# Optimization experiments

Hardware: AMD Instinct MI355X
Metric: run time of the kernel (lower is better)

Reference implementation:

```python
import jax, jax.numpy as jnp
import numpy as np

B, T, C = 4, 1024, 768
H, HS = 12, 64           # num_heads, head_size
VD = 2 * HS              # value dim per head


def setup_inputs() -> dict:
    key = jax.random.key(0)
    ks = jax.random.split(key, 16)
    s = 0.02
    inp = {
        "x": jax.random.normal(ks[0], (B, T, C), jnp.float32),
        "Wq1": jax.random.normal(ks[1], (H, C, HS), jnp.float32) * s,
        "Wk1": jax.random.normal(ks[2], (H, C, HS), jnp.float32) * s,
        "Wq2": jax.random.normal(ks[3], (H, C, HS), jnp.float32) * s,
        "Wk2": jax.random.normal(ks[4], (H, C, HS), jnp.float32) * s,
        "Wv": jax.random.normal(ks[5], (H, C, VD), jnp.float32) * s,
        "lq1": jax.random.normal(ks[6], (H, HS), jnp.float32) * 0.1,
        "lk1": jax.random.normal(ks[7], (H, HS), jnp.float32) * 0.1,
        "lq2": jax.random.normal(ks[8], (H, HS), jnp.float32) * 0.1,
        "lk2": jax.random.normal(ks[9], (H, HS), jnp.float32) * 0.1,
        "gn_w": jnp.ones((H * VD,), jnp.float32),
        "gn_b": jnp.zeros((H * VD,), jnp.float32),
        "Wp": jax.random.normal(ks[10], (C, H * VD), jnp.float32) * s,
        "bp": jnp.zeros((C,), jnp.float32),
        "layer_idx": 3,
    }
    return inp


def _diff_attn(x, Wq1, Wk1, Wq2, Wk2, Wv, lq1, lk1, lq2, lk2,
               gn_w, gn_b, Wp, bp, layer_idx):
    Bc, Tc, _ = x.shape
    scale = 1.0 / jnp.sqrt(jnp.float32(HS))
    # per-head projections: [B,H,T,HS]
    q1 = jnp.einsum('btc,hcd->bhtd', x, Wq1)
    k1 = jnp.einsum('btc,hcd->bhtd', x, Wk1)
    q2 = jnp.einsum('btc,hcd->bhtd', x, Wq2)
    k2 = jnp.einsum('btc,hcd->bhtd', x, Wk2)
    v = jnp.einsum('btc,hce->bhte', x, Wv)           # [B,H,T,2HS]
    mask = jnp.tril(jnp.ones((Tc, Tc), bool))         # causal
    neg = jnp.float32(-jnp.inf)
    a1 = jnp.einsum('bhtd,bhsd->bhts', q1, k1) * scale
    a2 = jnp.einsum('bhtd,bhsd->bhts', q2, k2) * scale
    a1 = jax.nn.softmax(jnp.where(mask, a1, neg), axis=-1)
    a2 = jax.nn.softmax(jnp.where(mask, a2, neg), axis=-1)
    # dynamic lambda init, per get_lambda
    li = jnp.float32(layer_idx)
    dyn = 0.8 - 0.6 * jnp.exp(-0.3 * (li - 1.0))
    lam = jnp.mean(jnp.exp(lq1 * lk1) - jnp.exp(lq2 * lk2) + dyn, axis=-1)  # [H]
    diff = a1 - lam[None, :, None, None] * a2
    out = jnp.einsum('bhts,bhse->bhte', diff, v)      # [B,H,T,2HS]
    out = out.transpose(0, 2, 1, 3).reshape(Bc, Tc, H * VD)
    # GroupLayerNorm == full layernorm over last dim (unbiased=False var)
    mu = out.mean(-1, keepdims=True)
    var = jnp.mean((out - mu) ** 2, axis=-1, keepdims=True)
    out = (out - mu) / jnp.sqrt(var + 1e-5) * gn_w + gn_b
    out = out * 0.2  # (1 - lambda_init_buffer=0.8), buffer never updated
    return out @ Wp.T + bp


def reference(x, Wq1, Wk1, Wq2, Wk2, Wv, lq1, lk1, lq2, lk2,
              gn_w, gn_b, Wp, bp, layer_idx):
    return _diff_attn(x, Wq1, Wk1, Wq2, Wk2, Wv, lq1, lk1, lq2, lk2,
                      gn_w, gn_b, Wp, bp, layer_idx)
```

## Files before the change

kernel.cpp:

```cpp
#include <hip/hip_runtime.h>
#include <hip/hip_bf16.h>

#define Bc   4
#define Tc   1024
#define Cc   768
#define Hc   12
#define HSc  64
#define VDc  128
#define NQKV 4608
#define YLD  3072
#define NROWS 4096
#define HVD  1536

#define Q1OFF 0
#define K1OFF 768
#define Q2OFF 1536
#define K2OFF 2304

typedef __bf16 bf16x8 __attribute__((ext_vector_type(8)));
typedef float f32x4 __attribute__((ext_vector_type(4)));

#define PW_S 36
#define EXP2SCALE 0.18033688011112042f

static __device__ __forceinline__ float bf2f(unsigned short s) {
    return __uint_as_float(((unsigned int)s) << 16);
}
static __device__ __forceinline__ unsigned short f2bf(float f) {
    unsigned int u = __float_as_uint(f);
    unsigned int r = (u + 0x7FFFu + ((u >> 16) & 1u)) >> 16;
    return (unsigned short)r;
}
static __device__ __forceinline__ unsigned int pack2bf(float lo, float hi) {
    unsigned int a = (__float_as_uint(lo) + 0x8000u) >> 16;
    unsigned int b = (__float_as_uint(hi) + 0x8000u) & 0xFFFF0000u;
    return a | b;
}

static __device__ __forceinline__ void load16_lds(const void* g, void* l) {
    __builtin_amdgcn_global_load_lds(
        (const __attribute__((address_space(1))) void*)g,
        (__attribute__((address_space(3))) void*)l, 16, 0, 0);
}

__global__ __launch_bounds__(256) void cast_bf16(
    const float* __restrict__ src, unsigned short* __restrict__ dst)
{
    int i = blockIdx.x * 256 + threadIdx.x;
    float4 v = *(const float4*)(src + (size_t)i * 4);
    ushort4 u;
    u.x = f2bf(v.x); u.y = f2bf(v.y); u.z = f2bf(v.z); u.w = f2bf(v.w);
    *(ushort4*)(dst + (size_t)i * 4) = u;
}

__global__ __launch_bounds__(256) void trans_w(
    const float* __restrict__ Wq1, const float* __restrict__ Wk1,
    const float* __restrict__ Wq2, const float* __restrict__ Wk2,
    const float* __restrict__ Wv, unsigned short* __restrict__ WcatT)
{
    __shared__ float tile[64][65];
    int tid = threadIdx.x;
    int t = blockIdx.x;
    int kt = t % 12, nt = t / 12;
    int k0 = kt * 64, n0 = nt * 64;
    const float* src;
    int stride;
    if (n0 < 3072) {
        int which = n0 / 768, m = n0 - which * 768, h = m >> 6;
        const float* W = (which == 0) ? Wq1 : (which == 1) ? Wk1 : (which == 2) ? Wq2 : Wk2;
        src = W + ((size_t)h * 768 + k0) * 64;
        stride = 64;
    } else {
        int rel = n0 - 3072, h = rel >> 7, e0 = rel & 127;
        src = Wv + ((size_t)h * 768 + k0) * 128 + e0;
        stride = 128;
    }
    for (int i = tid; i < 4096; i += 256) {
        int kl = i >> 6, dl = i & 63;
        tile[dl][kl] = src[(size_t)kl * stride + dl];
    }
    __syncthreads();
    for (int i = tid; i < 4096; i += 256) {
        int nl = i >> 6, kl = i & 63;
        WcatT[(size_t)(n0 + nl) * 768 + k0 + kl] = f2bf(tile[nl][kl]);
    }
}

__global__ __launch_bounds__(64) void lambda_kernel(
    const float* __restrict__ lq1, const float* __restrict__ lk1,
    const float* __restrict__ lq2, const float* __restrict__ lk2,
    const int* __restrict__ layer_idx, float* __restrict__ lam)
{
    int h = blockIdx.x, l = threadIdx.x;
    float li = (float)layer_idx[0];
    float dyn = 0.8f - 0.6f * expf(-0.3f * (li - 1.0f));
    int i = h * HSc + l;
    float v = expf(lq1[i] * lk1[i]) - expf(lq2[i] * lk2[i]) + dyn;
    #pragma unroll
    for (int off = 32; off; off >>= 1) v += __shfl_xor(v, off);
    if (l == 0) lam[h] = v * (1.0f / 64.0f);
}

template<int TN, int KD, int LDC, bool OUT_BIAS, bool SPLITV>
__global__ __launch_bounds__(256) void gemm_mfma(
    const unsigned short* __restrict__ A, const unsigned short* __restrict__ Bt,
    unsigned short* __restrict__ Cb, float* __restrict__ Cf,
    const float* __restrict__ bias, unsigned short* __restrict__ VtOut)
{
    constexpr int BN = TN * 32;
    constexpr int JB = TN / 2;
    __shared__ unsigned short As[128 * 32];
    __shared__ unsigned short Bs[BN * 32];
    int tid = threadIdx.x, lane = tid & 63, w = tid >> 6;
    int wm = w >> 1, wn = w & 1;
    int m0 = blockIdx.y * 128, n0 = blockIdx.x * BN;

    int lr = lane >> 2, lq = lane & 3;
    const unsigned short* gA[2];
    const unsigned short* gB[JB];
    #pragma unroll
    for (int j = 0; j < 2; ++j) {
        int row = w * 32 + j * 16 + lr;
        int qg = lq ^ ((row >> 1) & 3);
        gA[j] = A + (size_t)(m0 + row) * KD + qg * 8;
    }
    #pragma unroll
    for (int j = 0; j < JB; ++j) {
        int row = w * (JB * 16) + j * 16 + lr;
        int qg = lq ^ ((row >> 1) & 3);
        gB[j] = Bt + (size_t)(n0 + row) * KD + qg * 8;
    }

    int rr = lane & 15, qd = lane >> 4;
    const unsigned short* aAddr[4];
    const unsigned short* bAddr[TN];
    #pragma unroll
    for (int i = 0; i < 4; ++i) {
        int row = wm * 64 + i * 16 + rr;
        int qs = qd ^ ((row >> 1) & 3);
        aAddr[i] = As + row * 32 + qs * 8;
    }
    #pragma unroll
    for (int t = 0; t < TN; ++t) {
        int row = wn * (TN * 16) + t * 16 + rr;
        int qs = qd ^ ((row >> 1) & 3);
        bAddr[t] = Bs + row * 32 + qs * 8;
    }

    f32x4 acc[4][TN];
    #pragma unroll
    for (int i = 0; i < 4; ++i)
        #pragma unroll
        for (int t = 0; t < TN; ++t) acc[i][t] = {0.f, 0.f, 0.f, 0.f};

    for (int k = 0; k < KD / 32; ++k) {
        __syncthreads();
        load16_lds(gA[0], As + (w * 2 + 0) * 512);
        load16_lds(gA[1], As + (w * 2 + 1) * 512);
        #pragma unroll
        for (int j = 0; j < JB; ++j)
            load16_lds(gB[j], Bs + (w * JB + j) * 512);
        gA[0] += 32; gA[1] += 32;
        #pragma unroll
        for (int j = 0; j < JB; ++j) gB[j] += 32;
        __syncthreads();

        bf16x8 af[4], bfr[TN];
        #pragma unroll
        for (int i = 0; i < 4; ++i) af[i] = *(const bf16x8*)aAddr[i];
        #pragma unroll
        for (int t = 0; t < TN; ++t) bfr[t] = *(const bf16x8*)bAddr[t];
        #pragma unroll
        for (int i = 0; i < 4; ++i)
            #pragma unroll
            for (int t = 0; t < TN; ++t)
                acc[i][t] = __builtin_amdgcn_mfma_f32_16x16x32_bf16(af[i], bfr[t], acc[i][t], 0, 0, 0);
    }

    #pragma unroll
    for (int t = 0; t < TN; ++t) {
        int col = n0 + wn * (TN * 16) + t * 16 + rr;
        if (SPLITV && col >= 3072) {
            int rel = col - 3072, hh = rel >> 7, e = rel & 127;
            #pragma unroll
            for (int i = 0; i < 4; ++i) {
                int row0 = m0 + wm * 64 + i * 16 + qd * 4;
                int b = row0 >> 10, tt = row0 & 1023;
                ushort4 pk;
                pk.x = f2bf(acc[i][t][0]); pk.y = f2bf(acc[i][t][1]);
                pk.z = f2bf(acc[i][t][2]); pk.w = f2bf(acc[i][t][3]);
                *(ushort4*)&VtOut[(size_t)((b * Hc + hh) * 128 + e) * 1024 + tt] = pk;
            }
        } else {
            float bv = OUT_BIAS ? bias[col] : 0.f;
            #pragma unroll
            for (int i = 0; i < 4; ++i) {
                #pragma unroll
                for (int r = 0; r < 4; ++r) {
                    int row = m0 + wm * 64 + i * 16 + qd * 4 + r;
                    if (OUT_BIAS)
                        Cf[(size_t)row * LDC + col] = acc[i][t][r] + bv;
                    else
                        Cb[(size_t)row * LDC + col] = f2bf(acc[i][t][r]);
                }
            }
        }
    }
}

__global__ __launch_bounds__(256) void diff_attn_mfma(
    const unsigned short* __restrict__ Y, const unsigned short* __restrict__ Vt,
    const float* __restrict__ lam_buf, unsigned short* __restrict__ attn)
{
    __shared__ __align__(16) unsigned short KV[2][8192];
    __shared__ __align__(16) unsigned int PL32[4][16 * PW_S];

    int bh = blockIdx.x;
    int b = bh / Hc, h = bh - b * Hc;
    int g = 15 - (int)blockIdx.y;
    int tid = threadIdx.x, lane = tid & 63, wv = tid >> 6;
    int cl = lane & 15, qd = lane >> 4;
    float lamv = lam_buf[h];
    size_t rowbase = (size_t)(b * Tc) * YLD;
    const int hq = h * HSc;
    unsigned int* Pw = PL32[wv];
    const unsigned short* VtB = Vt + ((size_t)bh << 17);
    const f32x4 zero4 = {0.f, 0.f, 0.f, 0.f};

    int ksrow = lane >> 3;
    int ksch  = (lane & 7) ^ ksrow;
    int offk[4];
    {
        int mat = wv & 1;
        int moff = mat ? K2OFF : K1OFF;
        #pragma unroll
        for (int r8 = 0; r8 < 4; ++r8)
            offk[r8] = (r8 * 8 + ksrow) * YLD + moff + hq + ksch * 8;
    }
    int vsel = lane >> 2;
    int vsch = (lane & 3) ^ (vsel & 3);
    int offv[4];
    {
        int sv0 = (wv & 1) * 4;
        #pragma unroll
        for (int i = 0; i < 4; ++i)
            offv[i] = ((sv0 + i) * 16 + vsel) * 1024 + vsch * 8;
    }

    auto stage = [&](int kt, int cur) {
        char* base = (char*)KV[cur] + wv * 4096;
        if (wv < 2) {
            const unsigned short* g0 = Y + rowbase + (size_t)(kt * 32) * YLD;
            #pragma unroll
            for (int r8 = 0; r8 < 4; ++r8)
                load16_lds(g0 + offk[r8], base + r8 * 1024);
        } else {
            const unsigned short* g0 = VtB + kt * 32;
            #pragma unroll
            for (int i = 0; i < 4; ++i)
                load16_lds(g0 + offv[i], base + i * 1024);
        }
    };

    int kfo[2][4], vfo[8];
    #pragma unroll
    for (int c = 0; c < 2; ++c) {
        int row = c * 16 + cl;
        #pragma unroll
        for (int j = 0; j < 4; ++j)
            kfo[c][j] = (j >> 1) * 4096 + row * 128 +
                        ((((j & 1) * 4 + qd) ^ (row & 7)) << 4);
    }
    #pragma unroll
    for (int ec = 0; ec < 8; ++ec) {
        int e = ec * 16 + cl;
        vfo[ec] = 8192 + e * 64 + ((qd ^ (e & 3)) << 4);
    }

    int qrow = g * 64 + wv * 16;

    size_t qoff = rowbase + (size_t)(qrow + cl) * YLD;
    bf16x8 q1a = *(const bf16x8*)(Y + qoff + Q1OFF + hq + qd * 8);
    bf16x8 q1b = *(const bf16x8*)(Y + qoff + Q1OFF + hq + 32 + qd * 8);
    bf16x8 q2a = *(const bf16x8*)(Y + qoff + Q2OFF + hq + qd * 8);
    bf16x8 q2b = *(const bf16x8*)(Y + qoff + Q2OFF + hq + 32 + qd * 8);

    f32x4 O1[8], O2[8];
    #pragma unroll
    for (int ec = 0; ec < 8; ++ec) { O1[ec] = zero4; O2[ec] = zero4; }
    float l1[4] = {0.f, 0.f, 0.f, 0.f}, l2[4] = {0.f, 0.f, 0.f, 0.f};

    auto tile = [&](int cur, int kt, bool diag) {
        const char* kb = (const char*)KV[cur];
        bf16x8 kf[2][4];
        #pragma unroll
        for (int c = 0; c < 2; ++c)
            #pragma unroll
            for (int j = 0; j < 4; ++j)
                kf[c][j] = *(const bf16x8*)(kb + kfo[c][j]);

        f32x4 S1[2], S2[2];
        #pragma unroll
        for (int c = 0; c < 2; ++c) { S1[c] = zero4; S2[c] = zero4; }
        #pragma unroll
        for (int c = 0; c < 2; ++c) {
            S1[c] = __builtin_amdgcn_mfma_f32_16x16x32_bf16(q1a, kf[c][0], S1[c], 0, 0, 0);
            S1[c] = __builtin_amdgcn_mfma_f32_16x16x32_bf16(q1b, kf[c][1], S1[c], 0, 0, 0);
            S2[c] = __builtin_amdgcn_mfma_f32_16x16x32_bf16(q2a, kf[c][2], S2[c], 0, 0, 0);
            S2[c] = __builtin_amdgcn_mfma_f32_16x16x32_bf16(q2b, kf[c][3], S2[c], 0, 0, 0);
        }
        if (diag) {
            #pragma unroll
            for (int c = 0; c < 2; ++c) {
                int kq = kt * 32 + c * 16 + cl - qrow - qd * 4;
                #pragma unroll
                for (int r = 0; r < 4; ++r) {
                    if (kq > r) { S1[c][r] = -1e30f; S2[c][r] = -1e30f; }
                }
            }
        }
        bf16x8 vf[8];
        #pragma unroll
        for (int ec = 0; ec < 8; ++ec)
            vf[ec] = *(const bf16x8*)(kb + vfo[ec]);

        #pragma unroll
        for (int r = 0; r < 4; ++r) {
            float p10 = exp2f(S1[0][r] * EXP2SCALE);
            float p11 = exp2f(S1[1][r] * EXP2SCALE);
            float p20 = exp2f(S2[0][r] * EXP2SCALE);
            float p21 = exp2f(S2[1][r] * EXP2SCALE);
            l1[r] += p10 + p11;
            l2[r] += p20 + p21;
            int row = (qd << 2) + r;
            Pw[row * PW_S + cl]      = pack2bf(p10, p20);
            Pw[row * PW_S + cl + 16] = pack2bf(p11, p21);
        }
        const unsigned int* rp = Pw + cl * PW_S + qd * 8;
        uint4 L0 = *(const uint4*)(rp);
        uint4 L1 = *(const uint4*)(rp + 4);
        uint4 u1, u2;
        u1.x = __builtin_amdgcn_perm(L0.y, L0.x, 0x05040100u);
        u1.y = __builtin_amdgcn_perm(L0.w, L0.z, 0x05040100u);
        u1.z = __builtin_amdgcn_perm(L1.y, L1.x, 0x05040100u);
        u1.w = __builtin_amdgcn_perm(L1.w, L1.z, 0x05040100u);
        u2.x = __builtin_amdgcn_perm(L0.y, L0.x, 0x07060302u);
        u2.y = __builtin_amdgcn_perm(L0.w, L0.z, 0x07060302u);
        u2.z = __builtin_amdgcn_perm(L1.y, L1.x, 0x07060302u);
        u2.w = __builtin_amdgcn_perm(L1.w, L1.z, 0x07060302u);
        bf16x8 pa1 = __builtin_bit_cast(bf16x8, u1);
        bf16x8 pa2 = __builtin_bit_cast(bf16x8, u2);
        #pragma unroll
        for (int ec = 0; ec < 8; ++ec) {
            O1[ec] = __builtin_amdgcn_mfma_f32_16x16x32_bf16(pa1, vf[ec], O1[ec], 0, 0, 0);
            O2[ec] = __builtin_amdgcn_mfma_f32_16x16x32_bf16(pa2, vf[ec], O2[ec], 0, 0, 0);
        }
    };

    int NT = 2 * g + 2;
    int ktmax = 2 * g + (wv >> 1);

    stage(0, 0);
    __syncthreads();
    for (int kt = 0; kt < NT; ++kt) {
        int cur = kt & 1;
        if (kt + 1 < NT) stage(kt + 1, cur ^ 1);
        if (kt <= ktmax) {
            bool diag = (kt * 32 + 31 > qrow);
            tile(cur, kt, diag);
        }
        __syncthreads();
    }

    float w1[4], w2[4];
    #pragma unroll
    for (int r = 0; r < 4; ++r) {
        float a = l1[r], c = l2[r];
        a += __shfl_xor(a, 1); a += __shfl_xor(a, 2);
        a += __shfl_xor(a, 4); a += __shfl_xor(a, 8);
        c += __shfl_xor(c, 1); c += __shfl_xor(c, 2);
        c += __shfl_xor(c, 4); c += __shfl_xor(c, 8);
        w1[r] = 1.0f / a;
        w2[r] = lamv / c;
    }
    #pragma unroll
    for (int ec = 0; ec < 8; ++ec) {
        #pragma unroll
        for (int r = 0; r < 4; ++r) {
            size_t row = (size_t)(b * Tc + qrow + qd * 4 + r);
            attn[row * HVD + h * VDc + ec * 16 + cl] =
                f2bf(O1[ec][r] * w1[r] - O2[ec][r] * w2[r]);
        }
    }
}

__global__ __launch_bounds__(128) void ln_inplace(
    unsigned short* __restrict__ attn,
    const float* __restrict__ gnw, const float* __restrict__ gnb)
{
    int row = blockIdx.x, tid = threadIdx.x;
    unsigned short* p = attn + (size_t)row * HVD;
    float v[12];
    float s = 0.f, sq = 0.f;
    #pragma unroll
    for (int j = 0; j < 3; ++j) {
        int g = tid + j * 128;
        ushort4 u = *(const ushort4*)(p + g * 4);
        float x0 = bf2f(u.x), x1 = bf2f(u.y), x2 = bf2f(u.z), x3 = bf2f(u.w);
        v[j * 4 + 0] = x0; v[j * 4 + 1] = x1; v[j * 4 + 2] = x2; v[j * 4 + 3] = x3;
        s += x0 + x1 + x2 + x3;
        sq = fmaf(x0, x0, sq); sq = fmaf(x1, x1, sq);
        sq = fmaf(x2, x2, sq); sq = fmaf(x3, x3, sq);
    }
    #pragma unroll
    for (int off = 32; off; off >>= 1) { s += __shfl_xor(s, off); sq += __shfl_xor(sq, off); }
    __shared__ float ss[2], sqs[2];
    if ((tid & 63) == 0) { ss[tid >> 6] = s; sqs[tid >> 6] = sq; }
    __syncthreads();
    float S = ss[0] + ss[1], Q = sqs[0] + sqs[1];
    float mu = S * (1.0f / HVD);
    float rstd = rsqrtf(Q * (1.0f / HVD) - mu * mu + 1e-5f);
    #pragma unroll
    for (int j = 0; j < 3; ++j) {
        int g = tid + j * 128;
        float4 gw = *(const float4*)(gnw + g * 4);
        float4 gb = *(const float4*)(gnb + g * 4);
        ushort4 o;
        o.x = f2bf(((v[j * 4 + 0] - mu) * rstd * gw.x + gb.x) * 0.2f);
        o.y = f2bf(((v[j * 4 + 1] - mu) * rstd * gw.y + gb.y) * 0.2f);
        o.z = f2bf(((v[j * 4 + 2] - mu) * rstd * gw.z + gb.z) * 0.2f);
        o.w = f2bf(((v[j * 4 + 3] - mu) * rstd * gw.w + gb.w) * 0.2f);
        *(ushort4*)(p + g * 4) = o;
    }
}

extern "C" void kernel_launch(void* const* d_in, const int* in_sizes, int n_in,
                              void* d_out, int out_size, void* d_ws, size_t ws_size,
                              hipStream_t stream)
{
    const float* x   = (const float*)d_in[0];
    const float* Wq1 = (const float*)d_in[1];
    const float* Wk1 = (const float*)d_in[2];
    const float* Wq2 = (const float*)d_in[3];
    const float* Wk2 = (const float*)d_in[4];
    const float* Wv  = (const float*)d_in[5];
    const float* lq1 = (const float*)d_in[6];
    const float* lk1 = (const float*)d_in[7];
    const float* lq2 = (const float*)d_in[8];
    const float* lk2 = (const float*)d_in[9];
    const float* gnw = (const float*)d_in[10];
    const float* gnb = (const float*)d_in[11];
    const float* Wp  = (const float*)d_in[12];
    const float* bp  = (const float*)d_in[13];
    const int*   lidx = (const int*)d_in[14];
    float* out = (float*)d_out;

    char* w = (char*)d_ws;
    unsigned short* WcatT = (unsigned short*)(w);
    unsigned short* Xb    = (unsigned short*)(w + 7077888);
    unsigned short* Y     = (unsigned short*)(w + 13369344);
    unsigned short* VtW   = (unsigned short*)(w + 38535168);
    unsigned short* attn  = (unsigned short*)(w + 51118080);
    unsigned short* Wpb   = (unsigned short*)(w + 63700992);
    float* lam            = (float*)(w + 66060288);

    cast_bf16<<<dim3(NROWS * Cc / 1024), 256, 0, stream>>>(x, Xb);
    cast_bf16<<<dim3(Cc * HVD / 1024), 256, 0, stream>>>(Wp, Wpb);
    trans_w<<<dim3(72 * 12), 256, 0, stream>>>(Wq1, Wk1, Wq2, Wk2, Wv, WcatT);
    lambda_kernel<<<dim3(Hc), 64, 0, stream>>>(lq1, lk1, lq2, lk2, lidx, lam);
    gemm_mfma<4, 768, YLD, false, true><<<dim3(NQKV / 128, NROWS / 128), 256, 0, stream>>>(
        Xb, WcatT, Y, nullptr, nullptr, VtW);
    diff_attn_mfma<<<dim3(Bc * Hc, 16), 256, 0, stream>>>(Y, VtW, lam, attn);
    ln_inplace<<<dim3(NROWS), 128, 0, stream>>>(attn, gnw, gnb);
    gemm_mfma<2, HVD, Cc, true, false><<<dim3(Cc / 64, NROWS / 128), 256, 0, stream>>>(
        attn, Wpb, nullptr, out, bp, nullptr);
}
```

Baseline: 284.2 us.

## Triple-buffer K/V staging with single barrier and raw v_exp in diff attention

Replaces the double-buffered K/V LDS staging with a three-slot ring that prefetches two tiles ahead. Each iteration uses one explicit vmcnt wait plus s_barrier instead of two __syncthreads. K/V fragments are read into registers before the next stage is issued. The V swizzle pattern changes to reduce LDS bank conflicts, and exp2f is replaced with a raw v_exp_f32. The cost is more LDS per block, which may lower occupancy, and relying on hand-counted vmcnt values adds correctness risk.

```diff
diff --git a/kernel.cpp b/kernel.cpp
--- a/kernel.cpp
+++ b/kernel.cpp
@@ -19,6 +19,7 @@
 
 typedef __bf16 bf16x8 __attribute__((ext_vector_type(8)));
 typedef float f32x4 __attribute__((ext_vector_type(4)));
+typedef unsigned int u32x4 __attribute__((ext_vector_type(4)));
 
 #define PW_S 36
 #define EXP2SCALE 0.18033688011112042f
@@ -35,6 +36,11 @@
     unsigned int a = (__float_as_uint(lo) + 0x8000u) >> 16;
     unsigned int b = (__float_as_uint(hi) + 0x8000u) & 0xFFFF0000u;
     return a | b;
+}
+static __device__ __forceinline__ float fast_exp2(float x) {
+    float r;
+    asm("v_exp_f32 %0, %1" : "=v"(r) : "v"(x));
+    return r;
 }
 
 static __device__ __forceinline__ void load16_lds(const void* g, void* l) {
@@ -212,7 +218,7 @@
     const unsigned short* __restrict__ Y, const unsigned short* __restrict__ Vt,
     const float* __restrict__ lam_buf, unsigned short* __restrict__ attn)
 {
-    __shared__ __align__(16) unsigned short KV[2][8192];
+    __shared__ __align__(16) unsigned short KVring[3 * 8192];
     __shared__ __align__(16) unsigned int PL32[4][16 * PW_S];
 
     int bh = blockIdx.x;
@@ -238,7 +244,7 @@
             offk[r8] = (r8 * 8 + ksrow) * YLD + moff + hq + ksch * 8;
     }
     int vsel = lane >> 2;
-    int vsch = (lane & 3) ^ (vsel & 3);
+    int vsch = (lane & 3) ^ ((vsel >> 1) & 3);
     int offv[4];
     {
         int sv0 = (wv & 1) * 4;
@@ -247,8 +253,8 @@
             offv[i] = ((sv0 + i) * 16 + vsel) * 1024 + vsch * 8;
     }
 
-    auto stage = [&](int kt, int cur) {
-        char* base = (char*)KV[cur] + wv * 4096;
+    auto stage = [&](int kt, int slot) {
+        char* base = (char*)KVring + slot * 16384 + wv * 4096;
         if (wv < 2) {
             const unsigned short* g0 = Y + rowbase + (size_t)(kt * 32) * YLD;
             #pragma unroll
@@ -274,102 +280,114 @@
     #pragma unroll
     for (int ec = 0; ec < 8; ++ec) {
         int e = ec * 16 + cl;
-        vfo[ec] = 8192 + e * 64 + ((qd ^ (e & 3)) << 4);
+        vfo[ec] = 8192 + e * 64 + ((qd ^ ((e >> 1) & 3)) << 4);
     }
 
     int qrow = g * 64 + wv * 16;
 
     size_t qoff = rowbase + (size_t)(qrow + cl) * YLD;
-    bf16x8 q1a = *(const bf16x8*)(Y + qoff + Q1OFF + hq + qd * 8);
-    bf16x8 q1b = *(const bf16x8*)(Y + qoff + Q1OFF + hq + 32 + qd * 8);
-    bf16x8 q2a = *(const bf16x8*)(Y + qoff + Q2OFF + hq + qd * 8);
-    bf16x8 q2b = *(const bf16x8*)(Y + qoff + Q2OFF + hq + 32 + qd * 8);
+    u32x4 uq1a = *(const u32x4*)(Y + qoff + Q1OFF + hq + qd * 8);
+    u32x4 uq1b = *(const u32x4*)(Y + qoff + Q1OFF + hq + 32 + qd * 8);
+    u32x4 uq2a = *(const u32x4*)(Y + qoff + Q2OFF + hq + qd * 8);
+    u32x4 uq2b = *(const u32x4*)(Y + qoff + Q2OFF + hq + 32 + qd * 8);
+    asm volatile("" : "+v"(uq1a), "+v"(uq1b), "+v"(uq2a), "+v"(uq2b));
+    asm volatile("" : "+v"(lamv));
+    asm volatile("s_waitcnt vmcnt(0)" ::: "memory");
+    bf16x8 q1a = __builtin_bit_cast(bf16x8, uq1a);
+    bf16x8 q1b = __builtin_bit_cast(bf16x8, uq1b);
+    bf16x8 q2a = __builtin_bit_cast(bf16x8, uq2a);
+    bf16x8 q2b = __builtin_bit_cast(bf16x8, uq2b);
 
     f32x4 O1[8], O2[8];
     #pragma unroll
     for (int ec = 0; ec < 8; ++ec) { O1[ec] = zero4; O2[ec] = zero4; }
     float l1[4] = {0.f, 0.f, 0.f, 0.f}, l2[4] = {0.f, 0.f, 0.f, 0.f};
 
-    auto tile = [&](int cur, int kt, bool diag) {
-        const char* kb = (const char*)KV[cur];
+    int NT = 2 * g + 2;
+    int ktmax = 2 * g + (wv >> 1);
+
+    stage(0, 0);
+    stage(1, 1);
+
+    int cur = 0;
+    for (int kt = 0; kt < NT; ++kt) {
+        if (kt < NT - 1) {
+            asm volatile("s_waitcnt vmcnt(4)\n\ts_barrier" ::: "memory");
+        } else {
+            asm volatile("s_waitcnt vmcnt(0)\n\ts_barrier" ::: "memory");
+        }
+        const char* kb = (const char*)KVring + cur * 16384;
+
         bf16x8 kf[2][4];
         #pragma unroll
         for (int c = 0; c < 2; ++c)
             #pragma unroll
             for (int j = 0; j < 4; ++j)
                 kf[c][j] = *(const bf16x8*)(kb + kfo[c][j]);
-
-        f32x4 S1[2], S2[2];
-        #pragma unroll
-        for (int c = 0; c < 2; ++c) { S1[c] = zero4; S2[c] = zero4; }
-        #pragma unroll
-        for (int c = 0; c < 2; ++c) {
-            S1[c] = __builtin_amdgcn_mfma_f32_16x16x32_bf16(q1a, kf[c][0], S1[c], 0, 0, 0);
-            S1[c] = __builtin_amdgcn_mfma_f32_16x16x32_bf16(q1b, kf[c][1], S1[c], 0, 0, 0);
-            S2[c] = __builtin_amdgcn_mfma_f32_16x16x32_bf16(q2a, kf[c][2], S2[c], 0, 0, 0);
-            S2[c] = __builtin_amdgcn_mfma_f32_16x16x32_bf16(q2b, kf[c][3], S2[c], 0, 0, 0);
-        }
-        if (diag) {
-            #pragma unroll
-            for (int c = 0; c < 2; ++c) {
-                int kq = kt * 32 + c * 16 + cl - qrow - qd * 4;
-                #pragma unroll
-                for (int r = 0; r < 4; ++r) {
-                    if (kq > r) { S1[c][r] = -1e30f; S2[c][r] = -1e30f; }
-                }
-            }
-        }
         bf16x8 vf[8];
         #pragma unroll
         for (int ec = 0; ec < 8; ++ec)
             vf[ec] = *(const bf16x8*)(kb + vfo[ec]);
 
-        #pragma unroll
-        for (int r = 0; r < 4; ++r) {
-            float p10 = exp2f(S1[0][r] * EXP2SCALE);
-            float p11 = exp2f(S1[1][r] * EXP2SCALE);
-            float p20 = exp2f(S2[0][r] * EXP2SCALE);
-            float p21 = exp2f(S2[1][r] * EXP2SCALE);
-            l1[r] += p10 + p11;
-            l2[r] += p20 + p21;
-            int row = (qd << 2) + r;
-            Pw[row * PW_S + cl]      = pack2bf(p10, p20);
-            Pw[row * PW_S + cl + 16] = pack2bf(p11, p21);
-        }
-        const unsigned int* rp = Pw + cl * PW_S + qd * 8;
-        uint4 L0 = *(const uint4*)(rp);
-        uint4 L1 = *(const uint4*)(rp + 4);
-        uint4 u1, u2;
-        u1.x = __builtin_amdgcn_perm(L0.y, L0.x, 0x05040100u);
-        u1.y = __builtin_amdgcn_perm(L0.w, L0.z, 0x05040100u);
-        u1.z = __builtin_amdgcn_perm(L1.y, L1.x, 0x05040100u);
-        u1.w = __builtin_amdgcn_perm(L1.w, L1.z, 0x05040100u);
-        u2.x = __builtin_amdgcn_perm(L0.y, L0.x, 0x07060302u);
-        u2.y = __builtin_amdgcn_perm(L0.w, L0.z, 0x07060302u);
-        u2.z = __builtin_amdgcn_perm(L1.y, L1.x, 0x07060302u);
-        u2.w = __builtin_amdgcn_perm(L1.w, L1.z, 0x07060302u);
-        bf16x8 pa1 = __builtin_bit_cast(bf16x8, u1);
-        bf16x8 pa2 = __builtin_bit_cast(bf16x8, u2);
-        #pragma unroll
-        for (int ec = 0; ec < 8; ++ec) {
-            O1[ec] = __builtin_amdgcn_mfma_f32_16x16x32_bf16(pa1, vf[ec], O1[ec], 0, 0, 0);
-            O2[ec] = __builtin_amdgcn_mfma_f32_16x16x32_bf16(pa2, vf[ec], O2[ec], 0, 0, 0);
-        }
-    };
-
-    int NT = 2 * g + 2;
-    int ktmax = 2 * g + (wv >> 1);
-
-    stage(0, 0);
-    __syncthreads();
-    for (int kt = 0; kt < NT; ++kt) {
-        int cur = kt & 1;
-        if (kt + 1 < NT) stage(kt + 1, cur ^ 1);
+        if (kt + 2 < NT) {
+            int st = cur + 2; if (st >= 3) st -= 3;
+            stage(kt + 2, st);
+        }
+
         if (kt <= ktmax) {
-            bool diag = (kt * 32 + 31 > qrow);
-            tile(cur, kt, diag);
-        }
-        __syncthreads();
+            f32x4 S1[2], S2[2];
+            #pragma unroll
+            for (int c = 0; c < 2; ++c) { S1[c] = zero4; S2[c] = zero4; }
+            #pragma unroll
+            for (int c = 0; c < 2; ++c) {
+                S1[c] = __builtin_amdgcn_mfma_f32_16x16x32_bf16(q1a, kf[c][0], S1[c], 0, 0, 0);
+                S1[c] = __builtin_amdgcn_mfma_f32_16x16x32_bf16(q1b, kf[c][1], S1[c], 0, 0, 0);
+                S2[c] = __builtin_amdgcn_mfma_f32_16x16x32_bf16(q2a, kf[c][2], S2[c], 0, 0, 0);
+                S2[c] = __builtin_amdgcn_mfma_f32_16x16x32_bf16(q2b, kf[c][3], S2[c], 0, 0, 0);
+            }
+            if (kt * 32 + 31 > qrow) {
+                #pragma unroll
+                for (int c = 0; c < 2; ++c) {
+                    int kq = kt * 32 + c * 16 + cl - qrow - qd * 4;
+                    #pragma unroll
+                    for (int r = 0; r < 4; ++r) {
+                        if (kq > r) { S1[c][r] = -1e30f; S2[c][r] = -1e30f; }
+                    }
+                }
+            }
+            #pragma unroll
+            for (int r = 0; r < 4; ++r) {
+                float p10 = fast_exp2(S1[0][r] * EXP2SCALE);
+                float p11 = fast_exp2(S1[1][r] * EXP2SCALE);
+                float p20 = fast_exp2(S2[0][r] * EXP2SCALE);
+                float p21 = fast_exp2(S2[1][r] * EXP2SCALE);
+                l1[r] += p10 + p11;
+                l2[r] += p20 + p21;
+                int row = (qd << 2) + r;
+                Pw[row * PW_S + cl]      = pack2bf(p10, p20);
+                Pw[row * PW_S + cl + 16] = pack2bf(p11, p21);
+            }
+            const unsigned int* rp = Pw + cl * PW_S + qd * 8;
+            uint4 L0 = *(const uint4*)(rp);
+            uint4 L1 = *(const uint4*)(rp + 4);
+            uint4 u1, u2;
+            u1.x = __builtin_amdgcn_perm(L0.y, L0.x, 0x05040100u);
+            u1.y = __builtin_amdgcn_perm(L0.w, L0.z, 0x05040100u);
+            u1.z = __builtin_amdgcn_perm(L1.y, L1.x, 0x05040100u);
+            u1.w = __builtin_amdgcn_perm(L1.w, L1.z, 0x05040100u);
+            u2.x = __builtin_amdgcn_perm(L0.y, L0.x, 0x07060302u);
+            u2.y = __builtin_amdgcn_perm(L0.w, L0.z, 0x07060302u);
+            u2.z = __builtin_amdgcn_perm(L1.y, L1.x, 0x07060302u);
+            u2.w = __builtin_amdgcn_perm(L1.w, L1.z, 0x07060302u);
+            bf16x8 pa1 = __builtin_bit_cast(bf16x8, u1);
+            bf16x8 pa2 = __builtin_bit_cast(bf16x8, u2);
+            #pragma unroll
+            for (int ec = 0; ec < 8; ++ec) {
+                O1[ec] = __builtin_amdgcn_mfma_f32_16x16x32_bf16(pa1, vf[ec], O1[ec], 0, 0, 0);
+                O2[ec] = __builtin_amdgcn_mfma_f32_16x16x32_bf16(pa2, vf[ec], O2[ec], 0, 0, 0);
+            }
+        }
+        cur = (cur == 2) ? 0 : cur + 1;
     }
 
     float w1[4], w2[4];
```

New measurement: 280.1 us. No clear change (-1.4%).
